# Performance work log

Hardware: AMD Instinct MI355X
Metric: run time of the kernel (lower is better)

The kernel has to match this reference:

```python
import jax, jax.numpy as jnp
import numpy as np

B, N_PATCH, N_TABLE, N_CLS, E, H = 2, 2048, 16, 1, 512, 8
N = N_PATCH + N_TABLE + N_CLS  # 2065
D = E // H
SCALE = D ** -0.5
EPS = 1e-6


def setup_inputs() -> dict:
    key = jax.random.key(0)
    k0, k1, k2 = jax.random.split(key, 3)
    # 0.02 weight scale keeps A_raw moderate so the module's un-shifted exp() is stable,
    # matching typical trained-weight magnitudes.
    x = jax.random.normal(k0, (B, N, E), jnp.float32)
    w_qkv = jax.random.normal(k1, (E, 3 * E), jnp.float32) * 0.02
    b_qkv = jnp.zeros((3 * E,), jnp.float32)
    w_out = jax.random.normal(k2, (E, E), jnp.float32) * 0.02
    b_out = jnp.zeros((E,), jnp.float32)
    return {"x": x, "w_qkv": w_qkv, "b_qkv": b_qkv, "w_out": w_out, "b_out": b_out}


def _balanced_attention(A_raw):
    # Segmented softmax: patch / table / cls each normalized separately (no max-shift,
    # +1e-6 in denominator — faithful to the torch source), then mixed by a 3-way
    # softmax over (patch-mean, table-mean, cls-max) segment statistics.
    Ap = A_raw[..., :N_PATCH]
    At = A_raw[..., N_PATCH:N_PATCH + N_TABLE]
    Ac = A_raw[..., N_PATCH + N_TABLE:]
    ep = jnp.exp(Ap.mean(-1, keepdims=True))
    et = jnp.exp(At.mean(-1, keepdims=True))
    ec = jnp.exp(Ac.max(-1, keepdims=True))
    s = ep + et + ec
    def seg(a, w):
        e = jnp.exp(a)
        return e / (e.sum(-1, keepdims=True) + EPS) * w
    return jnp.concatenate([seg(Ap, ep / s), seg(At, et / s), seg(Ac, ec / s)], axis=-1)


def reference(x, w_qkv, b_qkv, w_out, b_out):
    qkv = x @ w_qkv + b_qkv                       # [B, N, 3E]
    q, k, v = jnp.split(qkv, 3, axis=-1)
    to_heads = lambda t: t.reshape(B, N, H, D).transpose(0, 2, 1, 3)  # b n (h d) -> b h n d
    q, k, v = to_heads(q), to_heads(k), to_heads(v)
    A_raw = jnp.einsum('bhnd,bhmd->bhnm', q, k) * SCALE
    A = _balanced_attention(A_raw)
    # dropout is identity in eval mode
    out = jnp.einsum('bhnm,bhmd->bhnd', A, v)
    out = out.transpose(0, 2, 1, 3).reshape(B, N, E)  # b h n d -> b n (h d)
    out = out @ w_out + b_out
    return (out, A, A_raw)
```

## Files before the change

kernel.cpp:

```cpp
#include <hip/hip_runtime.h>
#include <hip/hip_bf16.h>

#define BB     2
#define NN     2065
#define NPAD   2112
#define HH     8
#define DD     64
#define EE     512
#define MROWS  (BB*NN)
#define NPATCH 2048
#define NTAB   16
#define SCALEF 0.125f
#define EPSF   1e-6f

typedef __bf16 bf16;
typedef bf16  bf16x8 __attribute__((ext_vector_type(8)));
typedef bf16  bf16x4v __attribute__((ext_vector_type(4)));
typedef float f32x4  __attribute__((ext_vector_type(4)));

#define LDS_STRIDE 72

__global__ __launch_bounds__(256) void k_zero(uint4* __restrict__ p, int n4) {
    int i = blockIdx.x * 256 + threadIdx.x;
    if (i < n4) { uint4 z = {0,0,0,0}; p[i] = z; }
}

__global__ __launch_bounds__(256) void k_cvt(const float* __restrict__ x,
                                             bf16* __restrict__ o, int n4) {
    int i = blockIdx.x * 256 + threadIdx.x;
    if (i < n4) {
        float4 v = ((const float4*)x)[i];
        bf16x4v r;
        r[0] = (bf16)v.x; r[1] = (bf16)v.y; r[2] = (bf16)v.z; r[3] = (bf16)v.w;
        *(bf16x4v*)(o + 4*(size_t)i) = r;
    }
}

__global__ __launch_bounds__(256) void k_transcvt(const float* __restrict__ w,
                                                  bf16* __restrict__ o,
                                                  int C, int total) {
    int i = blockIdx.x * 256 + threadIdx.x;
    if (i < total) {
        int k = i & 511, c = i >> 9;
        o[i] = (bf16)w[(size_t)k * C + c];
    }
}

__global__ __launch_bounds__(256) void k_gemm_qkv(
    const bf16* __restrict__ xb, const bf16* __restrict__ wt,
    const float* __restrict__ bias,
    bf16* __restrict__ Qh, bf16* __restrict__ Kh, bf16* __restrict__ Vt)
{
    __shared__ bf16 As[64][LDS_STRIDE];
    __shared__ bf16 Bs[64][LDS_STRIDE];
    int t = threadIdx.x;
    int w = t >> 6, l = t & 63, l15 = l & 15, quad = l >> 4;
    int m0 = blockIdx.y * 64, c0 = blockIdx.x * 64;
    int srow = t >> 2, sseg = (t & 3) * 16;
    f32x4 acc[4] = {};

    for (int kk = 0; kk < 512; kk += 64) {
        {
            int m = m0 + srow;
            uint4 v0 = {0,0,0,0}, v1 = {0,0,0,0};
            if (m < MROWS) {
                const uint4* src = (const uint4*)(xb + (size_t)m*512 + kk + sseg);
                v0 = src[0]; v1 = src[1];
            }
            *(uint4*)&As[srow][sseg]     = v0;
            *(uint4*)&As[srow][sseg + 8] = v1;
            const uint4* bs = (const uint4*)(wt + (size_t)(c0 + srow)*512 + kk + sseg);
            *(uint4*)&Bs[srow][sseg]     = bs[0];
            *(uint4*)&Bs[srow][sseg + 8] = bs[1];
        }
        __syncthreads();
        #pragma unroll
        for (int kh = 0; kh < 2; kh++) {
            bf16x8 a = *(const bf16x8*)&As[w*16 + l15][kh*32 + quad*8];
            #pragma unroll
            for (int c = 0; c < 4; c++) {
                bf16x8 b = *(const bf16x8*)&Bs[c*16 + l15][kh*32 + quad*8];
                acc[c] = __builtin_amdgcn_mfma_f32_16x16x32_bf16(a, b, acc[c], 0, 0, 0);
            }
        }
        __syncthreads();
    }

    int which = c0 >> 9;
    int h = (c0 & 511) >> 6;
    #pragma unroll
    for (int c = 0; c < 4; c++) {
        int d  = (c0 & 63) + c*16 + l15;
        float bv = bias[c0 + c*16 + l15];
        #pragma unroll
        for (int r = 0; r < 4; r++) {
            int m = m0 + w*16 + quad*4 + r;
            if (m >= MROWS) continue;
            int b_ = m / NN, n = m - b_ * NN;
            int bh = b_ * 8 + h;
            float v = acc[c][r] + bv;
            if (which == 0)      Qh[(size_t)(bh*NPAD + n)*64 + d] = (bf16)v;
            else if (which == 1) Kh[(size_t)(bh*NPAD + n)*64 + d] = (bf16)v;
            else                 Vt[((size_t)bh*64 + d)*NPAD + n] = (bf16)v;
        }
    }
}

__global__ __launch_bounds__(256) void k_attn1(
    const bf16* __restrict__ Qh, const bf16* __restrict__ Kh,
    float* __restrict__ Araw, float4* __restrict__ stats)
{
    __shared__ bf16 Qs[64][LDS_STRIDE];
    __shared__ bf16 Ks[64][LDS_STRIDE];
    int t = threadIdx.x;
    int w = t >> 6, l = t & 63, l15 = l & 15, quad = l >> 4;
    int n0 = blockIdx.x * 64;
    int bh = blockIdx.y;
    int srow = t >> 2, sseg = (t & 3) * 16;
    {
        const uint4* src = (const uint4*)(Qh + (size_t)(bh*NPAD + n0 + srow)*64 + sseg);
        *(uint4*)&Qs[srow][sseg]     = src[0];
        *(uint4*)&Qs[srow][sseg + 8] = src[1];
    }
    float sp[4]  = {0,0,0,0}, sep[4] = {0,0,0,0};
    float st[4]  = {0,0,0,0}, set_[4] = {0,0,0,0}, cv[4] = {0,0,0,0};
    int nrow[4];
    #pragma unroll
    for (int r = 0; r < 4; r++) nrow[r] = n0 + w*16 + quad*4 + r;

    for (int kt = 0; kt < 33; kt++) {
        __syncthreads();
        {
            const uint4* src = (const uint4*)(Kh + (size_t)(bh*NPAD + kt*64 + srow)*64 + sseg);
            *(uint4*)&Ks[srow][sseg]     = src[0];
            *(uint4*)&Ks[srow][sseg + 8] = src[1];
        }
        __syncthreads();
        f32x4 acc[4] = {};
        #pragma unroll
        for (int kh = 0; kh < 2; kh++) {
            bf16x8 a = *(const bf16x8*)&Qs[w*16 + l15][kh*32 + quad*8];
            #pragma unroll
            for (int c = 0; c < 4; c++) {
                bf16x8 b = *(const bf16x8*)&Ks[c*16 + l15][kh*32 + quad*8];
                acc[c] = __builtin_amdgcn_mfma_f32_16x16x32_bf16(a, b, acc[c], 0, 0, 0);
            }
        }
        #pragma unroll
        for (int c = 0; c < 4; c++) {
            int col = kt*64 + c*16 + l15;
            #pragma unroll
            for (int r = 0; r < 4; r++) {
                float val = acc[c][r] * SCALEF;
                float e = __expf(val);
                if (col < NPATCH)            { sp[r] += val; sep[r] += e; }
                else if (col < NPATCH+NTAB)  { st[r] += val; set_[r] += e; }
                else if (col == NPATCH+NTAB) { cv[r] = val; }
                if (col < NN && nrow[r] < NN)
                    Araw[((size_t)(bh*NN + nrow[r]))*NN + col] = val;
            }
        }
    }
    #pragma unroll
    for (int r = 0; r < 4; r++) {
        #pragma unroll
        for (int m = 1; m < 16; m <<= 1) {
            sp[r]   += __shfl_xor(sp[r],   m, 64);
            sep[r]  += __shfl_xor(sep[r],  m, 64);
            st[r]   += __shfl_xor(st[r],   m, 64);
            set_[r] += __shfl_xor(set_[r], m, 64);
            cv[r]   += __shfl_xor(cv[r],   m, 64);
        }
    }
    if (l15 == 0) {
        #pragma unroll
        for (int r = 0; r < 4; r++) {
            if (nrow[r] < NN) {
                float ep = __expf(sp[r] * (1.0f / NPATCH));
                float et = __expf(st[r] * (1.0f / NTAB));
                float ec = __expf(cv[r]);
                float s  = ep + et + ec;
                float4 o;
                o.x = ep / (s * (sep[r]  + EPSF));
                o.y = et / (s * (set_[r] + EPSF));
                o.z = ec / (s * (ec      + EPSF));
                o.w = 0.f;
                stats[bh*NPAD + nrow[r]] = o;
            }
        }
    }
}

__global__ __launch_bounds__(256) void k_attn2(
    const bf16* __restrict__ Qh, const bf16* __restrict__ Kh,
    const bf16* __restrict__ Vt, const float4* __restrict__ stats,
    float* __restrict__ A, bf16* __restrict__ attn)
{
    __shared__ bf16 Qs[64][LDS_STRIDE];
    __shared__ bf16 Ks[64][LDS_STRIDE];
    __shared__ bf16 Vs[64][LDS_STRIDE];
    __shared__ bf16 Ps[64][LDS_STRIDE];
    int t = threadIdx.x;
    int w = t >> 6, l = t & 63, l15 = l & 15, quad = l >> 4;
    int n0 = blockIdx.x * 64;
    int bh = blockIdx.y;
    int srow = t >> 2, sseg = (t & 3) * 16;
    {
        const uint4* src = (const uint4*)(Qh + (size_t)(bh*NPAD + n0 + srow)*64 + sseg);
        *(uint4*)&Qs[srow][sseg]     = src[0];
        *(uint4*)&Qs[srow][sseg + 8] = src[1];
    }
    int nrow[4];
    float cp[4], ctb[4], cc[4];
    #pragma unroll
    for (int r = 0; r < 4; r++) {
        nrow[r] = n0 + w*16 + quad*4 + r;
        float4 s4 = stats[bh*NPAD + nrow[r]];
        cp[r] = s4.x; ctb[r] = s4.y; cc[r] = s4.z;
    }
    f32x4 o[4] = {};

    for (int kt = 0; kt < 33; kt++) {
        __syncthreads();
        {
            const uint4* ks = (const uint4*)(Kh + (size_t)(bh*NPAD + kt*64 + srow)*64 + sseg);
            *(uint4*)&Ks[srow][sseg]     = ks[0];
            *(uint4*)&Ks[srow][sseg + 8] = ks[1];
            const uint4* vs = (const uint4*)(Vt + ((size_t)bh*64 + srow)*NPAD + kt*64 + sseg);
            *(uint4*)&Vs[srow][sseg]     = vs[0];
            *(uint4*)&Vs[srow][sseg + 8] = vs[1];
        }
        __syncthreads();
        f32x4 acc[4] = {};
        #pragma unroll
        for (int kh = 0; kh < 2; kh++) {
            bf16x8 a = *(const bf16x8*)&Qs[w*16 + l15][kh*32 + quad*8];
            #pragma unroll
            for (int c = 0; c < 4; c++) {
                bf16x8 b = *(const bf16x8*)&Ks[c*16 + l15][kh*32 + quad*8];
                acc[c] = __builtin_amdgcn_mfma_f32_16x16x32_bf16(a, b, acc[c], 0, 0, 0);
            }
        }
        #pragma unroll
        for (int c = 0; c < 4; c++) {
            int col = kt*64 + c*16 + l15;
            #pragma unroll
            for (int r = 0; r < 4; r++) {
                float val = acc[c][r] * SCALEF;
                float e = __expf(val);
                float coef = (col < NPATCH) ? cp[r]
                           : (col < NPATCH+NTAB) ? ctb[r]
                           : (col == NPATCH+NTAB) ? cc[r] : 0.f;
                float av = e * coef;
                if (col < NN && nrow[r] < NN)
                    A[((size_t)(bh*NN + nrow[r]))*NN + col] = av;
                Ps[w*16 + quad*4 + r][c*16 + l15] = (bf16)av;
            }
        }
        __syncthreads();
        #pragma unroll
        for (int kh = 0; kh < 2; kh++) {
            bf16x8 pa = *(const bf16x8*)&Ps[w*16 + l15][kh*32 + quad*8];
            #pragma unroll
            for (int g = 0; g < 4; g++) {
                bf16x8 vb = *(const bf16x8*)&Vs[g*16 + l15][kh*32 + quad*8];
                o[g] = __builtin_amdgcn_mfma_f32_16x16x32_bf16(pa, vb, o[g], 0, 0, 0);
            }
        }
    }
    int b_ = bh >> 3, h = bh & 7;
    #pragma unroll
    for (int g = 0; g < 4; g++) {
        #pragma unroll
        for (int r = 0; r < 4; r++) {
            int n = nrow[r];
            if (n < NN)
                attn[((size_t)(b_*NN + n))*512 + h*64 + g*16 + l15] = (bf16)o[g][r];
        }
    }
}

__global__ __launch_bounds__(256) void k_gemm_out(
    const bf16* __restrict__ attn, const bf16* __restrict__ wt,
    const float* __restrict__ bias, float* __restrict__ out)
{
    __shared__ bf16 As[64][LDS_STRIDE];
    __shared__ bf16 Bs[64][LDS_STRIDE];
    int t = threadIdx.x;
    int w = t >> 6, l = t & 63, l15 = l & 15, quad = l >> 4;
    int m0 = blockIdx.y * 64, c0 = blockIdx.x * 64;
    int srow = t >> 2, sseg = (t & 3) * 16;
    f32x4 acc[4] = {};

    for (int kk = 0; kk < 512; kk += 64) {
        {
            int m = m0 + srow;
            uint4 v0 = {0,0,0,0}, v1 = {0,0,0,0};
            if (m < MROWS) {
                const uint4* src = (const uint4*)(attn + (size_t)m*512 + kk + sseg);
                v0 = src[0]; v1 = src[1];
            }
            *(uint4*)&As[srow][sseg]     = v0;
            *(uint4*)&As[srow][sseg + 8] = v1;
            const uint4* bs = (const uint4*)(wt + (size_t)(c0 + srow)*512 + kk + sseg);
            *(uint4*)&Bs[srow][sseg]     = bs[0];
            *(uint4*)&Bs[srow][sseg + 8] = bs[1];
        }
        __syncthreads();
        #pragma unroll
        for (int kh = 0; kh < 2; kh++) {
            bf16x8 a = *(const bf16x8*)&As[w*16 + l15][kh*32 + quad*8];
            #pragma unroll
            for (int c = 0; c < 4; c++) {
                bf16x8 b = *(const bf16x8*)&Bs[c*16 + l15][kh*32 + quad*8];
                acc[c] = __builtin_amdgcn_mfma_f32_16x16x32_bf16(a, b, acc[c], 0, 0, 0);
            }
        }
        __syncthreads();
    }
    #pragma unroll
    for (int c = 0; c < 4; c++) {
        int col = c0 + c*16 + l15;
        float bv = bias[col];
        #pragma unroll
        for (int r = 0; r < 4; r++) {
            int m = m0 + w*16 + quad*4 + r;
            if (m < MROWS)
                out[(size_t)m*512 + col] = acc[c][r] + bv;
        }
    }
}

extern "C" void kernel_launch(void* const* d_in, const int* in_sizes, int n_in,
                              void* d_out, int out_size, void* d_ws, size_t ws_size,
                              hipStream_t stream)
{
    const float* x     = (const float*)d_in[0];
    const float* w_qkv = (const float*)d_in[1];
    const float* b_qkv = (const float*)d_in[2];
    const float* w_out = (const float*)d_in[3];
    const float* b_out = (const float*)d_in[4];

    float* out  = (float*)d_out;
    float* A    = out + (size_t)MROWS * 512;
    float* Araw = A   + (size_t)BB * HH * NN * NN;

    char* ws = (char*)d_ws;
    size_t off = 0;
    auto alloc = [&](size_t bytes) {
        char* p = ws + off;
        off += (bytes + 255) & ~(size_t)255;
        return p;
    };
    bf16*  xb    = (bf16*)alloc((size_t)MROWS * 512 * 2);
    bf16*  wqt   = (bf16*)alloc((size_t)1536 * 512 * 2);
    bf16*  wot   = (bf16*)alloc((size_t)512 * 512 * 2);
    bf16*  Qh    = (bf16*)alloc((size_t)16 * NPAD * 64 * 2);
    bf16*  Kh    = (bf16*)alloc((size_t)16 * NPAD * 64 * 2);
    bf16*  Vt    = (bf16*)alloc((size_t)16 * NPAD * 64 * 2);
    float4* stats = (float4*)alloc((size_t)16 * NPAD * 16);
    bf16*  attn  = (bf16*)alloc((size_t)MROWS * 512 * 2);
    (void)ws_size; (void)in_sizes; (void)n_in; (void)out_size;

    int zero4 = (int)((size_t)3 * 16 * NPAD * 64 * 2 / 16);
    k_zero<<<dim3((zero4 + 255) / 256), 256, 0, stream>>>((uint4*)Qh, zero4);

    k_cvt<<<dim3((MROWS*512/4 + 255) / 256), 256, 0, stream>>>(x, xb, MROWS*512/4);
    k_transcvt<<<dim3(1536*512/256), 256, 0, stream>>>(w_qkv, wqt, 1536, 1536*512);
    k_transcvt<<<dim3(512*512/256),  256, 0, stream>>>(w_out, wot, 512,  512*512);

    k_gemm_qkv<<<dim3(24, 65), 256, 0, stream>>>(xb, wqt, b_qkv, Qh, Kh, Vt);
    k_attn1<<<dim3(33, 16), 256, 0, stream>>>(Qh, Kh, Araw, stats);
    k_attn2<<<dim3(33, 16), 256, 0, stream>>>(Qh, Kh, Vt, stats, A, attn);
    k_gemm_out<<<dim3(8, 65), 256, 0, stream>>>(attn, wot, b_out, out);
}
```

Measured before the change: 729.7 us.

## Fuse two-pass attention into one kernel holding full score rows in registers

Merges the stats pass and the probability/PV pass into one kernel. Each block now handles 16 query rows, and each wave owns a quarter of the key range. The QK^T scores stay in registers (33 accumulators per thread), so QK^T is no longer computed twice and the stats buffer round-trip goes away. Segment statistics are reduced across waves through LDS. The normalized probabilities for the whole row are then staged in LDS, and each wave computes 16 output dims of P@V. This costs heavy register pressure and large LDS per block, and the key and value loads are per-wave with little reuse across query rows.

```diff
diff --git a/kernel.cpp b/kernel.cpp
--- a/kernel.cpp
+++ b/kernel.cpp
@@ -106,177 +106,158 @@
     }
 }
 
-__global__ __launch_bounds__(256) void k_attn1(
+__global__ __launch_bounds__(256, 2) void k_attn_fused(
     const bf16* __restrict__ Qh, const bf16* __restrict__ Kh,
-    float* __restrict__ Araw, float4* __restrict__ stats)
+    const bf16* __restrict__ Vt,
+    float* __restrict__ Araw, float* __restrict__ A,
+    bf16* __restrict__ attn)
 {
-    __shared__ bf16 Qs[64][LDS_STRIDE];
-    __shared__ bf16 Ks[64][LDS_STRIDE];
+    __shared__ bf16 Ps[16][2120];
+    __shared__ bf16 Kw[4][16][LDS_STRIDE];
+    __shared__ float sSP[4][16], sSE[4][16];
+    __shared__ float sT[16], sTE[16], sC[16];
+
     int t = threadIdx.x;
     int w = t >> 6, l = t & 63, l15 = l & 15, quad = l >> 4;
-    int n0 = blockIdx.x * 64;
+    int n0 = blockIdx.x * 16;
     int bh = blockIdx.y;
-    int srow = t >> 2, sseg = (t & 3) * 16;
-    {
-        const uint4* src = (const uint4*)(Qh + (size_t)(bh*NPAD + n0 + srow)*64 + sseg);
-        *(uint4*)&Qs[srow][sseg]     = src[0];
-        *(uint4*)&Qs[srow][sseg + 8] = src[1];
-    }
-    float sp[4]  = {0,0,0,0}, sep[4] = {0,0,0,0};
-    float st[4]  = {0,0,0,0}, set_[4] = {0,0,0,0}, cv[4] = {0,0,0,0};
-    int nrow[4];
-    #pragma unroll
-    for (int r = 0; r < 4; r++) nrow[r] = n0 + w*16 + quad*4 + r;
-
-    for (int kt = 0; kt < 33; kt++) {
-        __syncthreads();
-        {
-            const uint4* src = (const uint4*)(Kh + (size_t)(bh*NPAD + kt*64 + srow)*64 + sseg);
-            *(uint4*)&Ks[srow][sseg]     = src[0];
-            *(uint4*)&Ks[srow][sseg + 8] = src[1];
-        }
-        __syncthreads();
-        f32x4 acc[4] = {};
-        #pragma unroll
-        for (int kh = 0; kh < 2; kh++) {
-            bf16x8 a = *(const bf16x8*)&Qs[w*16 + l15][kh*32 + quad*8];
+    int lrow = l >> 2, lseg = (l & 3) * 16;
+
+    const bf16* qrow = Qh + ((size_t)bh * NPAD + n0 + l15) * 64 + quad * 8;
+    bf16x8 qa0 = *(const bf16x8*)qrow;
+    bf16x8 qa1 = *(const bf16x8*)(qrow + 32);
+
+    const bf16* kbase = Kh + ((size_t)bh * NPAD + w * 528) * 64;
+    const uint4* kp = (const uint4*)(kbase + (size_t)lrow * 64 + lseg);
+    uint4 p0 = kp[0], p1 = kp[1];
+
+    f32x4 acc[33];
+    float sp[4] = {0,0,0,0}, sep[4] = {0,0,0,0};
+    float st[4] = {0,0,0,0}, set_[4] = {0,0,0,0}, cv[4] = {0,0,0,0};
+
+    #pragma unroll
+    for (int kt = 0; kt < 33; ++kt) {
+        *(uint4*)&Kw[w][lrow][lseg]     = p0;
+        *(uint4*)&Kw[w][lrow][lseg + 8] = p1;
+        if (kt < 32) {
+            const uint4* np = (const uint4*)(kbase + ((size_t)(kt+1)*16 + lrow) * 64 + lseg);
+            p0 = np[0]; p1 = np[1];
+        }
+        bf16x8 b0 = *(const bf16x8*)&Kw[w][l15][quad*8];
+        bf16x8 b1 = *(const bf16x8*)&Kw[w][l15][32 + quad*8];
+        f32x4 c = {0,0,0,0};
+        c = __builtin_amdgcn_mfma_f32_16x16x32_bf16(qa0, b0, c, 0, 0, 0);
+        c = __builtin_amdgcn_mfma_f32_16x16x32_bf16(qa1, b1, c, 0, 0, 0);
+        #pragma unroll
+        for (int r = 0; r < 4; ++r) {
+            float val = c[r] * SCALEF;
+            c[r] = val;
+            if (w < 3 || kt <= 28)      { sp[r] += val; sep[r]  += __expf(val); }
+            else if (kt == 29)          { st[r] += val; set_[r] += __expf(val); }
+            else if (kt == 30)          { if (l15 == 0) cv[r] = val; }
+        }
+        acc[kt] = c;
+    }
+
+    #pragma unroll
+    for (int r = 0; r < 4; ++r) {
+        #pragma unroll
+        for (int m = 1; m < 16; m <<= 1) {
+            sp[r]  += __shfl_xor(sp[r],  m, 64);
+            sep[r] += __shfl_xor(sep[r], m, 64);
+        }
+    }
+    if (w == 3) {
+        #pragma unroll
+        for (int r = 0; r < 4; ++r) {
             #pragma unroll
-            for (int c = 0; c < 4; c++) {
-                bf16x8 b = *(const bf16x8*)&Ks[c*16 + l15][kh*32 + quad*8];
-                acc[c] = __builtin_amdgcn_mfma_f32_16x16x32_bf16(a, b, acc[c], 0, 0, 0);
-            }
-        }
-        #pragma unroll
-        for (int c = 0; c < 4; c++) {
-            int col = kt*64 + c*16 + l15;
-            #pragma unroll
-            for (int r = 0; r < 4; r++) {
-                float val = acc[c][r] * SCALEF;
-                float e = __expf(val);
-                if (col < NPATCH)            { sp[r] += val; sep[r] += e; }
-                else if (col < NPATCH+NTAB)  { st[r] += val; set_[r] += e; }
-                else if (col == NPATCH+NTAB) { cv[r] = val; }
-                if (col < NN && nrow[r] < NN)
-                    Araw[((size_t)(bh*NN + nrow[r]))*NN + col] = val;
-            }
-        }
-    }
-    #pragma unroll
-    for (int r = 0; r < 4; r++) {
-        #pragma unroll
-        for (int m = 1; m < 16; m <<= 1) {
-            sp[r]   += __shfl_xor(sp[r],   m, 64);
-            sep[r]  += __shfl_xor(sep[r],  m, 64);
-            st[r]   += __shfl_xor(st[r],   m, 64);
-            set_[r] += __shfl_xor(set_[r], m, 64);
-            cv[r]   += __shfl_xor(cv[r],   m, 64);
+            for (int m = 1; m < 16; m <<= 1) {
+                st[r]   += __shfl_xor(st[r],   m, 64);
+                set_[r] += __shfl_xor(set_[r], m, 64);
+                cv[r]   += __shfl_xor(cv[r],   m, 64);
+            }
         }
     }
     if (l15 == 0) {
         #pragma unroll
-        for (int r = 0; r < 4; r++) {
-            if (nrow[r] < NN) {
-                float ep = __expf(sp[r] * (1.0f / NPATCH));
-                float et = __expf(st[r] * (1.0f / NTAB));
-                float ec = __expf(cv[r]);
-                float s  = ep + et + ec;
-                float4 o;
-                o.x = ep / (s * (sep[r]  + EPSF));
-                o.y = et / (s * (set_[r] + EPSF));
-                o.z = ec / (s * (ec      + EPSF));
-                o.w = 0.f;
-                stats[bh*NPAD + nrow[r]] = o;
-            }
-        }
-    }
-}
-
-__global__ __launch_bounds__(256) void k_attn2(
-    const bf16* __restrict__ Qh, const bf16* __restrict__ Kh,
-    const bf16* __restrict__ Vt, const float4* __restrict__ stats,
-    float* __restrict__ A, bf16* __restrict__ attn)
-{
-    __shared__ bf16 Qs[64][LDS_STRIDE];
-    __shared__ bf16 Ks[64][LDS_STRIDE];
-    __shared__ bf16 Vs[64][LDS_STRIDE];
-    __shared__ bf16 Ps[64][LDS_STRIDE];
-    int t = threadIdx.x;
-    int w = t >> 6, l = t & 63, l15 = l & 15, quad = l >> 4;
-    int n0 = blockIdx.x * 64;
-    int bh = blockIdx.y;
-    int srow = t >> 2, sseg = (t & 3) * 16;
-    {
-        const uint4* src = (const uint4*)(Qh + (size_t)(bh*NPAD + n0 + srow)*64 + sseg);
-        *(uint4*)&Qs[srow][sseg]     = src[0];
-        *(uint4*)&Qs[srow][sseg + 8] = src[1];
-    }
-    int nrow[4];
-    float cp[4], ctb[4], cc[4];
-    #pragma unroll
-    for (int r = 0; r < 4; r++) {
-        nrow[r] = n0 + w*16 + quad*4 + r;
-        float4 s4 = stats[bh*NPAD + nrow[r]];
-        cp[r] = s4.x; ctb[r] = s4.y; cc[r] = s4.z;
-    }
-    f32x4 o[4] = {};
-
-    for (int kt = 0; kt < 33; kt++) {
-        __syncthreads();
-        {
-            const uint4* ks = (const uint4*)(Kh + (size_t)(bh*NPAD + kt*64 + srow)*64 + sseg);
-            *(uint4*)&Ks[srow][sseg]     = ks[0];
-            *(uint4*)&Ks[srow][sseg + 8] = ks[1];
-            const uint4* vs = (const uint4*)(Vt + ((size_t)bh*64 + srow)*NPAD + kt*64 + sseg);
-            *(uint4*)&Vs[srow][sseg]     = vs[0];
-            *(uint4*)&Vs[srow][sseg + 8] = vs[1];
-        }
-        __syncthreads();
-        f32x4 acc[4] = {};
-        #pragma unroll
-        for (int kh = 0; kh < 2; kh++) {
-            bf16x8 a = *(const bf16x8*)&Qs[w*16 + l15][kh*32 + quad*8];
-            #pragma unroll
-            for (int c = 0; c < 4; c++) {
-                bf16x8 b = *(const bf16x8*)&Ks[c*16 + l15][kh*32 + quad*8];
-                acc[c] = __builtin_amdgcn_mfma_f32_16x16x32_bf16(a, b, acc[c], 0, 0, 0);
-            }
-        }
-        #pragma unroll
-        for (int c = 0; c < 4; c++) {
-            int col = kt*64 + c*16 + l15;
-            #pragma unroll
-            for (int r = 0; r < 4; r++) {
-                float val = acc[c][r] * SCALEF;
-                float e = __expf(val);
-                float coef = (col < NPATCH) ? cp[r]
-                           : (col < NPATCH+NTAB) ? ctb[r]
-                           : (col == NPATCH+NTAB) ? cc[r] : 0.f;
-                float av = e * coef;
-                if (col < NN && nrow[r] < NN)
-                    A[((size_t)(bh*NN + nrow[r]))*NN + col] = av;
-                Ps[w*16 + quad*4 + r][c*16 + l15] = (bf16)av;
-            }
-        }
-        __syncthreads();
-        #pragma unroll
-        for (int kh = 0; kh < 2; kh++) {
-            bf16x8 pa = *(const bf16x8*)&Ps[w*16 + l15][kh*32 + quad*8];
-            #pragma unroll
-            for (int g = 0; g < 4; g++) {
-                bf16x8 vb = *(const bf16x8*)&Vs[g*16 + l15][kh*32 + quad*8];
-                o[g] = __builtin_amdgcn_mfma_f32_16x16x32_bf16(pa, vb, o[g], 0, 0, 0);
-            }
-        }
+        for (int r = 0; r < 4; ++r) {
+            sSP[w][quad*4 + r] = sp[r];
+            sSE[w][quad*4 + r] = sep[r];
+            if (w == 3) {
+                sT [quad*4 + r] = st[r];
+                sTE[quad*4 + r] = set_[r];
+                sC [quad*4 + r] = cv[r];
+            }
+        }
+    }
+    __syncthreads();
+
+    float cp[4], ct[4], cc[4];
+    #pragma unroll
+    for (int r = 0; r < 4; ++r) {
+        int row = quad*4 + r;
+        float spt  = sSP[0][row] + sSP[1][row] + sSP[2][row] + sSP[3][row];
+        float sept = sSE[0][row] + sSE[1][row] + sSE[2][row] + sSE[3][row];
+        float ep = __expf(spt * (1.0f / NPATCH));
+        float et = __expf(sT[row] * (1.0f / NTAB));
+        float ec = __expf(sC[row]);
+        float s  = ep + et + ec;
+        cp[r] = ep / (s * (sept     + EPSF));
+        ct[r] = et / (s * (sTE[row] + EPSF));
+        cc[r] = ec / (s * (ec       + EPSF));
+    }
+
+    int nvalid[4]; size_t rb[4];
+    #pragma unroll
+    for (int r = 0; r < 4; ++r) {
+        int n = n0 + quad*4 + r;
+        nvalid[r] = (n < NN);
+        rb[r] = ((size_t)(bh * NN + n)) * NN;
+    }
+    #pragma unroll
+    for (int kt = 0; kt < 33; ++kt) {
+        int colbase = w * 528 + kt * 16 + l15;
+        #pragma unroll
+        for (int r = 0; r < 4; ++r) {
+            float val = acc[kt][r];
+            float av; bool stok;
+            if (w < 3 || kt <= 28) { av = __expf(val) * cp[r]; stok = true; }
+            else if (kt == 29)     { av = __expf(val) * ct[r]; stok = true; }
+            else if (kt == 30)     { av = (l15 == 0) ? __expf(val) * cc[r] : 0.f; stok = (l15 == 0); }
+            else                   { av = 0.f; stok = false; }
+            Ps[quad*4 + r][colbase] = (bf16)av;
+            if (stok && nvalid[r]) {
+                Araw[rb[r] + colbase] = val;
+                A   [rb[r] + colbase] = av;
+            }
+        }
+    }
+    __syncthreads();
+
+    const bf16* vbase = Vt + ((size_t)bh * 64 + w * 16) * NPAD;
+    const uint4* vp = (const uint4*)(vbase + (size_t)lrow * NPAD + lseg);
+    uint4 v0 = vp[0], v1 = vp[1];
+    f32x4 o = {0,0,0,0};
+    for (int nt = 0; nt < 33; ++nt) {
+        *(uint4*)&Kw[w][lrow][lseg]     = v0;
+        *(uint4*)&Kw[w][lrow][lseg + 8] = v1;
+        if (nt < 32) {
+            const uint4* np = (const uint4*)(vbase + (size_t)lrow * NPAD + (nt+1)*64 + lseg);
+            v0 = np[0]; v1 = np[1];
+        }
+        bf16x8 pa0 = *(const bf16x8*)&Ps[l15][nt*64 + quad*8];
+        bf16x8 pa1 = *(const bf16x8*)&Ps[l15][nt*64 + 32 + quad*8];
+        bf16x8 vb0 = *(const bf16x8*)&Kw[w][l15][quad*8];
+        bf16x8 vb1 = *(const bf16x8*)&Kw[w][l15][32 + quad*8];
+        o = __builtin_amdgcn_mfma_f32_16x16x32_bf16(pa0, vb0, o, 0, 0, 0);
+        o = __builtin_amdgcn_mfma_f32_16x16x32_bf16(pa1, vb1, o, 0, 0, 0);
     }
     int b_ = bh >> 3, h = bh & 7;
     #pragma unroll
-    for (int g = 0; g < 4; g++) {
-        #pragma unroll
-        for (int r = 0; r < 4; r++) {
-            int n = nrow[r];
-            if (n < NN)
-                attn[((size_t)(b_*NN + n))*512 + h*64 + g*16 + l15] = (bf16)o[g][r];
-        }
+    for (int r = 0; r < 4; ++r) {
+        int n = n0 + quad*4 + r;
+        if (n < NN)
+            attn[((size_t)(b_ * NN + n)) * 512 + h * 64 + w * 16 + l15] = (bf16)o[r];
     }
 }
 
@@ -358,7 +339,6 @@
     bf16*  Qh    = (bf16*)alloc((size_t)16 * NPAD * 64 * 2);
     bf16*  Kh    = (bf16*)alloc((size_t)16 * NPAD * 64 * 2);
     bf16*  Vt    = (bf16*)alloc((size_t)16 * NPAD * 64 * 2);
-    float4* stats = (float4*)alloc((size_t)16 * NPAD * 16);
     bf16*  attn  = (bf16*)alloc((size_t)MROWS * 512 * 2);
     (void)ws_size; (void)in_sizes; (void)n_in; (void)out_size;
 
@@ -370,7 +350,6 @@
     k_transcvt<<<dim3(512*512/256),  256, 0, stream>>>(w_out, wot, 512,  512*512);
 
     k_gemm_qkv<<<dim3(24, 65), 256, 0, stream>>>(xb, wqt, b_qkv, Qh, Kh, Vt);
-    k_attn1<<<dim3(33, 16), 256, 0, stream>>>(Qh, Kh, Araw, stats);
-    k_attn2<<<dim3(33, 16), 256, 0, stream>>>(Qh, Kh, Vt, stats, A, attn);
+    k_attn_fused<<<dim3(130, 16), 256, 0, stream>>>(Qh, Kh, Vt, Araw, A, attn);
     k_gemm_out<<<dim3(8, 65), 256, 0, stream>>>(attn, wot, b_out, out);
 }
```

Result: slower. 818.5 us (+12.2%).

## Reuse Araw in second attention pass and load K/V fragments directly to registers

Applied to the files above, without the earlier changes.

The second attention kernel no longer recomputes QK^T. It reads the already-written fp32 Araw matrix back from global memory, exponentiates and scales it to produce A and P, and double-buffers P in LDS so each iteration needs one barrier instead of three. Both attention kernels drop LDS staging of Q/K/V and load MFMA fragments straight from global memory into registers, with software prefetch of the next tile. This trades MFMA work and barriers for an extra large fp32 read of Araw (about 136MB) plus uncoalesced register-direct loads. There is also a read-after-write dependency on Araw across kernels.

```diff
diff --git a/kernel.cpp b/kernel.cpp
--- a/kernel.cpp
+++ b/kernel.cpp
@@ -106,63 +106,76 @@
     }
 }
 
+#define A1_LOADK(dst, ktv) do {                                                    \
+    const bf16* kbn_ = kb + (size_t)(ktv)*4096;                                    \
+    _Pragma("unroll")                                                              \
+    for (int c = 0; c < 4; ++c) {                                                  \
+        dst[2*c]   = *(const bf16x8*)(kbn_ + c*1024);                              \
+        dst[2*c+1] = *(const bf16x8*)(kbn_ + c*1024 + 32);                         \
+    }                                                                              \
+} while (0)
+
+#define A1_BODY(ktv, kf) do {                                                      \
+    f32x4 acc_[4] = {};                                                            \
+    _Pragma("unroll")                                                              \
+    for (int c = 0; c < 4; ++c) {                                                  \
+        acc_[c] = __builtin_amdgcn_mfma_f32_16x16x32_bf16(qa0, kf[2*c],   acc_[c], 0, 0, 0); \
+        acc_[c] = __builtin_amdgcn_mfma_f32_16x16x32_bf16(qa1, kf[2*c+1], acc_[c], 0, 0, 0); \
+    }                                                                              \
+    _Pragma("unroll")                                                              \
+    for (int c = 0; c < 4; ++c) {                                                  \
+        int col_ = (ktv)*64 + c*16 + l15;                                          \
+        bool vc_ = col_ < NN;                                                      \
+        _Pragma("unroll")                                                          \
+        for (int r = 0; r < 4; ++r) {                                              \
+            float val_ = acc_[c][r] * SCALEF;                                      \
+            float e_ = __expf(val_);                                               \
+            if (col_ < NPATCH)            { sp[r] += val_; sep[r]  += e_; }        \
+            else if (col_ < NPATCH+NTAB)  { st[r] += val_; set_[r] += e_; }        \
+            else if (col_ == NPATCH+NTAB) { cv[r] = val_; }                        \
+            if (vc_ && vr[r]) Araw[rbase[r] + col_] = val_;                        \
+        }                                                                          \
+    }                                                                              \
+} while (0)
+
 __global__ __launch_bounds__(256) void k_attn1(
     const bf16* __restrict__ Qh, const bf16* __restrict__ Kh,
     float* __restrict__ Araw, float4* __restrict__ stats)
 {
-    __shared__ bf16 Qs[64][LDS_STRIDE];
-    __shared__ bf16 Ks[64][LDS_STRIDE];
     int t = threadIdx.x;
     int w = t >> 6, l = t & 63, l15 = l & 15, quad = l >> 4;
     int n0 = blockIdx.x * 64;
     int bh = blockIdx.y;
-    int srow = t >> 2, sseg = (t & 3) * 16;
-    {
-        const uint4* src = (const uint4*)(Qh + (size_t)(bh*NPAD + n0 + srow)*64 + sseg);
-        *(uint4*)&Qs[srow][sseg]     = src[0];
-        *(uint4*)&Qs[srow][sseg + 8] = src[1];
-    }
-    float sp[4]  = {0,0,0,0}, sep[4] = {0,0,0,0};
+
+    const bf16* qp = Qh + ((size_t)(bh*NPAD) + n0 + w*16 + l15)*64 + quad*8;
+    bf16x8 qa0 = *(const bf16x8*)qp;
+    bf16x8 qa1 = *(const bf16x8*)(qp + 32);
+
+    const bf16* kb = Kh + (size_t)(bh*NPAD)*64 + (size_t)(l15*64) + quad*8;
+
+    int nrow[4]; bool vr[4]; size_t rbase[4];
+    #pragma unroll
+    for (int r = 0; r < 4; ++r) {
+        nrow[r] = n0 + w*16 + quad*4 + r;
+        vr[r] = nrow[r] < NN;
+        rbase[r] = ((size_t)(bh*NN + nrow[r]))*NN;
+    }
+
+    float sp[4]  = {0,0,0,0}, sep[4]  = {0,0,0,0};
     float st[4]  = {0,0,0,0}, set_[4] = {0,0,0,0}, cv[4] = {0,0,0,0};
-    int nrow[4];
-    #pragma unroll
-    for (int r = 0; r < 4; r++) nrow[r] = n0 + w*16 + quad*4 + r;
-
-    for (int kt = 0; kt < 33; kt++) {
-        __syncthreads();
-        {
-            const uint4* src = (const uint4*)(Kh + (size_t)(bh*NPAD + kt*64 + srow)*64 + sseg);
-            *(uint4*)&Ks[srow][sseg]     = src[0];
-            *(uint4*)&Ks[srow][sseg + 8] = src[1];
-        }
-        __syncthreads();
-        f32x4 acc[4] = {};
-        #pragma unroll
-        for (int kh = 0; kh < 2; kh++) {
-            bf16x8 a = *(const bf16x8*)&Qs[w*16 + l15][kh*32 + quad*8];
-            #pragma unroll
-            for (int c = 0; c < 4; c++) {
-                bf16x8 b = *(const bf16x8*)&Ks[c*16 + l15][kh*32 + quad*8];
-                acc[c] = __builtin_amdgcn_mfma_f32_16x16x32_bf16(a, b, acc[c], 0, 0, 0);
-            }
-        }
-        #pragma unroll
-        for (int c = 0; c < 4; c++) {
-            int col = kt*64 + c*16 + l15;
-            #pragma unroll
-            for (int r = 0; r < 4; r++) {
-                float val = acc[c][r] * SCALEF;
-                float e = __expf(val);
-                if (col < NPATCH)            { sp[r] += val; sep[r] += e; }
-                else if (col < NPATCH+NTAB)  { st[r] += val; set_[r] += e; }
-                else if (col == NPATCH+NTAB) { cv[r] = val; }
-                if (col < NN && nrow[r] < NN)
-                    Araw[((size_t)(bh*NN + nrow[r]))*NN + col] = val;
-            }
-        }
-    }
-    #pragma unroll
-    for (int r = 0; r < 4; r++) {
+
+    bf16x8 kc[8], kn[8];
+    A1_LOADK(kc, 0);
+    for (int kt = 0; kt < 32; kt += 2) {
+        A1_LOADK(kn, kt + 1);
+        A1_BODY(kt, kc);
+        A1_LOADK(kc, kt + 2);
+        A1_BODY(kt + 1, kn);
+    }
+    A1_BODY(32, kc);
+
+    #pragma unroll
+    for (int r = 0; r < 4; ++r) {
         #pragma unroll
         for (int m = 1; m < 16; m <<= 1) {
             sp[r]   += __shfl_xor(sp[r],   m, 64);
@@ -174,7 +187,7 @@
     }
     if (l15 == 0) {
         #pragma unroll
-        for (int r = 0; r < 4; r++) {
+        for (int r = 0; r < 4; ++r) {
             if (nrow[r] < NN) {
                 float ep = __expf(sp[r] * (1.0f / NPATCH));
                 float et = __expf(st[r] * (1.0f / NTAB));
@@ -191,88 +204,91 @@
     }
 }
 
+#define A2_LOADV(dst, ktv) do {                                                    \
+    _Pragma("unroll")                                                              \
+    for (int c = 0; c < 4; ++c) {                                                  \
+        int col_ = (ktv)*64 + c*16 + l15;                                          \
+        bool vc_ = col_ < NN;                                                      \
+        _Pragma("unroll")                                                          \
+        for (int r = 0; r < 4; ++r)                                                \
+            dst[c*4+r] = (vc_ && vr[r]) ? Araw[rbase[r] + col_] : 0.f;             \
+    }                                                                              \
+} while (0)
+
+#define A2_BODY(ktv, vvv) do {                                                     \
+    int buf_ = (ktv) & 1;                                                          \
+    _Pragma("unroll")                                                              \
+    for (int c = 0; c < 4; ++c) {                                                  \
+        int col_ = (ktv)*64 + c*16 + l15;                                          \
+        bool vc_ = col_ < NN;                                                      \
+        _Pragma("unroll")                                                          \
+        for (int r = 0; r < 4; ++r) {                                              \
+            float av_ = 0.f;                                                       \
+            if (vc_ && vr[r]) {                                                    \
+                float coef_ = (col_ < NPATCH) ? cp[r]                              \
+                            : (col_ < NPATCH+NTAB) ? ct4[r] : cc4[r];              \
+                av_ = __expf(vvv[c*4+r]) * coef_;                                  \
+                A[rbase[r] + col_] = av_;                                          \
+            }                                                                      \
+            Ps[buf_][w*16 + quad*4 + r][c*16 + l15] = (bf16)av_;                   \
+        }                                                                          \
+    }                                                                              \
+    __syncthreads();                                                               \
+    {                                                                              \
+        bf16x8 pa0_ = *(const bf16x8*)&Ps[buf_][w*16 + l15][quad*8];               \
+        bf16x8 pa1_ = *(const bf16x8*)&Ps[buf_][w*16 + l15][32 + quad*8];          \
+        _Pragma("unroll")                                                          \
+        for (int g = 0; g < 4; ++g) {                                              \
+            bf16x8 v0_ = *(const bf16x8*)(vb + (size_t)(g*16)*NPAD + (ktv)*64);    \
+            bf16x8 v1_ = *(const bf16x8*)(vb + (size_t)(g*16)*NPAD + (ktv)*64 + 32); \
+            o[g] = __builtin_amdgcn_mfma_f32_16x16x32_bf16(pa0_, v0_, o[g], 0, 0, 0); \
+            o[g] = __builtin_amdgcn_mfma_f32_16x16x32_bf16(pa1_, v1_, o[g], 0, 0, 0); \
+        }                                                                          \
+    }                                                                              \
+} while (0)
+
 __global__ __launch_bounds__(256) void k_attn2(
-    const bf16* __restrict__ Qh, const bf16* __restrict__ Kh,
-    const bf16* __restrict__ Vt, const float4* __restrict__ stats,
+    const float* __restrict__ Araw, const float4* __restrict__ stats,
+    const bf16* __restrict__ Vt,
     float* __restrict__ A, bf16* __restrict__ attn)
 {
-    __shared__ bf16 Qs[64][LDS_STRIDE];
-    __shared__ bf16 Ks[64][LDS_STRIDE];
-    __shared__ bf16 Vs[64][LDS_STRIDE];
-    __shared__ bf16 Ps[64][LDS_STRIDE];
+    __shared__ bf16 Ps[2][64][LDS_STRIDE];
     int t = threadIdx.x;
     int w = t >> 6, l = t & 63, l15 = l & 15, quad = l >> 4;
     int n0 = blockIdx.x * 64;
     int bh = blockIdx.y;
-    int srow = t >> 2, sseg = (t & 3) * 16;
-    {
-        const uint4* src = (const uint4*)(Qh + (size_t)(bh*NPAD + n0 + srow)*64 + sseg);
-        *(uint4*)&Qs[srow][sseg]     = src[0];
-        *(uint4*)&Qs[srow][sseg + 8] = src[1];
-    }
-    int nrow[4];
-    float cp[4], ctb[4], cc[4];
-    #pragma unroll
-    for (int r = 0; r < 4; r++) {
+
+    int nrow[4]; bool vr[4]; size_t rbase[4];
+    float cp[4], ct4[4], cc4[4];
+    #pragma unroll
+    for (int r = 0; r < 4; ++r) {
         nrow[r] = n0 + w*16 + quad*4 + r;
-        float4 s4 = stats[bh*NPAD + nrow[r]];
-        cp[r] = s4.x; ctb[r] = s4.y; cc[r] = s4.z;
-    }
+        vr[r] = nrow[r] < NN;
+        rbase[r] = ((size_t)(bh*NN + nrow[r]))*NN;
+        float4 s4 = {0.f, 0.f, 0.f, 0.f};
+        if (vr[r]) s4 = stats[bh*NPAD + nrow[r]];
+        cp[r] = s4.x; ct4[r] = s4.y; cc4[r] = s4.z;
+    }
+
+    const bf16* vb = Vt + (size_t)(bh*64)*NPAD + (size_t)(l15)*NPAD + quad*8;
+
     f32x4 o[4] = {};
-
-    for (int kt = 0; kt < 33; kt++) {
-        __syncthreads();
-        {
-            const uint4* ks = (const uint4*)(Kh + (size_t)(bh*NPAD + kt*64 + srow)*64 + sseg);
-            *(uint4*)&Ks[srow][sseg]     = ks[0];
-            *(uint4*)&Ks[srow][sseg + 8] = ks[1];
-            const uint4* vs = (const uint4*)(Vt + ((size_t)bh*64 + srow)*NPAD + kt*64 + sseg);
-            *(uint4*)&Vs[srow][sseg]     = vs[0];
-            *(uint4*)&Vs[srow][sseg + 8] = vs[1];
-        }
-        __syncthreads();
-        f32x4 acc[4] = {};
-        #pragma unroll
-        for (int kh = 0; kh < 2; kh++) {
-            bf16x8 a = *(const bf16x8*)&Qs[w*16 + l15][kh*32 + quad*8];
-            #pragma unroll
-            for (int c = 0; c < 4; c++) {
-                bf16x8 b = *(const bf16x8*)&Ks[c*16 + l15][kh*32 + quad*8];
-                acc[c] = __builtin_amdgcn_mfma_f32_16x16x32_bf16(a, b, acc[c], 0, 0, 0);
-            }
-        }
-        #pragma unroll
-        for (int c = 0; c < 4; c++) {
-            int col = kt*64 + c*16 + l15;
-            #pragma unroll
-            for (int r = 0; r < 4; r++) {
-                float val = acc[c][r] * SCALEF;
-                float e = __expf(val);
-                float coef = (col < NPATCH) ? cp[r]
-                           : (col < NPATCH+NTAB) ? ctb[r]
-                           : (col == NPATCH+NTAB) ? cc[r] : 0.f;
-                float av = e * coef;
-                if (col < NN && nrow[r] < NN)
-                    A[((size_t)(bh*NN + nrow[r]))*NN + col] = av;
-                Ps[w*16 + quad*4 + r][c*16 + l15] = (bf16)av;
-            }
-        }
-        __syncthreads();
-        #pragma unroll
-        for (int kh = 0; kh < 2; kh++) {
-            bf16x8 pa = *(const bf16x8*)&Ps[w*16 + l15][kh*32 + quad*8];
-            #pragma unroll
-            for (int g = 0; g < 4; g++) {
-                bf16x8 vb = *(const bf16x8*)&Vs[g*16 + l15][kh*32 + quad*8];
-                o[g] = __builtin_amdgcn_mfma_f32_16x16x32_bf16(pa, vb, o[g], 0, 0, 0);
-            }
-        }
-    }
+    float vv[16], nv[16];
+
+    A2_LOADV(vv, 0);
+    for (int kt = 0; kt < 32; kt += 2) {
+        A2_LOADV(nv, kt + 1);
+        A2_BODY(kt, vv);
+        A2_LOADV(vv, kt + 2);
+        A2_BODY(kt + 1, nv);
+    }
+    A2_BODY(32, vv);
+
     int b_ = bh >> 3, h = bh & 7;
     #pragma unroll
-    for (int g = 0; g < 4; g++) {
-        #pragma unroll
-        for (int r = 0; r < 4; r++) {
+    for (int g = 0; g < 4; ++g) {
+        #pragma unroll
+        for (int r = 0; r < 4; ++r) {
             int n = nrow[r];
             if (n < NN)
                 attn[((size_t)(b_*NN + n))*512 + h*64 + g*16 + l15] = (bf16)o[g][r];
@@ -371,6 +387,6 @@
 
     k_gemm_qkv<<<dim3(24, 65), 256, 0, stream>>>(xb, wqt, b_qkv, Qh, Kh, Vt);
     k_attn1<<<dim3(33, 16), 256, 0, stream>>>(Qh, Kh, Araw, stats);
-    k_attn2<<<dim3(33, 16), 256, 0, stream>>>(Qh, Kh, Vt, stats, A, attn);
+    k_attn2<<<dim3(33, 16), 256, 0, stream>>>(Araw, stats, Vt, A, attn);
     k_gemm_out<<<dim3(8, 65), 256, 0, stream>>>(attn, wot, b_out, out);
 }
```

Result: slower. 991.2 us (+35.8%).

## Read stored raw scores in attn2 instead of recomputing QK^T, with prefetch

Applied to the files above, without the earlier changes.

The second attention pass no longer reloads Q and K or recomputes QK^T with MFMA. It reads the fp32 A_raw already written by the first pass, applies exp and the segment coefficients, and writes A. A and V tiles are register-prefetched one tile ahead to overlap global loads with compute. This trades MFMA work for an extra read of the large fp32 A_raw matrix (about 136MB). The kernel is memory-bound either way, so the net effect depends on the cache hitting the just-written A_raw.

```diff
diff --git a/kernel.cpp b/kernel.cpp
--- a/kernel.cpp
+++ b/kernel.cpp
@@ -17,6 +17,8 @@
 typedef bf16  bf16x8 __attribute__((ext_vector_type(8)));
 typedef bf16  bf16x4v __attribute__((ext_vector_type(4)));
 typedef float f32x4  __attribute__((ext_vector_type(4)));
+
+struct __attribute__((packed, aligned(4))) f4p { float v[4]; };
 
 #define LDS_STRIDE 72
 
@@ -192,70 +194,104 @@
 }
 
 __global__ __launch_bounds__(256) void k_attn2(
-    const bf16* __restrict__ Qh, const bf16* __restrict__ Kh,
-    const bf16* __restrict__ Vt, const float4* __restrict__ stats,
+    const float* __restrict__ Araw, const float4* __restrict__ stats,
+    const bf16* __restrict__ Vt,
     float* __restrict__ A, bf16* __restrict__ attn)
 {
-    __shared__ bf16 Qs[64][LDS_STRIDE];
-    __shared__ bf16 Ks[64][LDS_STRIDE];
+    __shared__ bf16 Ps[64][LDS_STRIDE];
     __shared__ bf16 Vs[64][LDS_STRIDE];
-    __shared__ bf16 Ps[64][LDS_STRIDE];
+    __shared__ float sCp[64], sCt[64], sCc[64];
+
     int t = threadIdx.x;
     int w = t >> 6, l = t & 63, l15 = l & 15, quad = l >> 4;
     int n0 = blockIdx.x * 64;
     int bh = blockIdx.y;
-    int srow = t >> 2, sseg = (t & 3) * 16;
-    {
-        const uint4* src = (const uint4*)(Qh + (size_t)(bh*NPAD + n0 + srow)*64 + sseg);
-        *(uint4*)&Qs[srow][sseg]     = src[0];
-        *(uint4*)&Qs[srow][sseg + 8] = src[1];
-    }
-    int nrow[4];
-    float cp[4], ctb[4], cc[4];
-    #pragma unroll
-    for (int r = 0; r < 4; r++) {
-        nrow[r] = n0 + w*16 + quad*4 + r;
-        float4 s4 = stats[bh*NPAD + nrow[r]];
-        cp[r] = s4.x; ctb[r] = s4.y; cc[r] = s4.z;
-    }
+    int pr = t >> 2;
+    int ps = (t & 3) * 16;
+
+    if (t < 64) {
+        bool v = (n0 + t) < NN;
+        float4 s4 = {0.f, 0.f, 0.f, 0.f};
+        if (v) s4 = stats[bh*NPAD + n0 + t];
+        sCp[t] = v ? s4.x : 0.f;
+        sCt[t] = v ? s4.y : 0.f;
+        sCc[t] = v ? s4.z : 0.f;
+    }
+    __syncthreads();
+    float cpr = sCp[pr], ctr = sCt[pr], ccr = sCc[pr];
+
+    bool prv = (n0 + pr) < NN;
+    size_t arow = ((size_t)(bh*NN) + n0 + pr) * NN;
+    const bf16* vrow = Vt + ((size_t)(bh*64) + pr) * NPAD;
+
+#define LOAD_A(dst, ktv) do {                                                  \
+    _Pragma("unroll")                                                          \
+    for (int j = 0; j < 4; ++j) {                                              \
+        int c0_ = (ktv)*64 + ps + j*4;                                         \
+        f4p v_ = {{0.f, 0.f, 0.f, 0.f}};                                       \
+        if (prv) {                                                             \
+            if (c0_ + 3 < NN) v_ = *(const f4p*)(Araw + arow + c0_);           \
+            else {                                                             \
+                if (c0_     < NN) v_.v[0] = Araw[arow + c0_];                  \
+                if (c0_ + 1 < NN) v_.v[1] = Araw[arow + c0_ + 1];              \
+                if (c0_ + 2 < NN) v_.v[2] = Araw[arow + c0_ + 2];              \
+                if (c0_ + 3 < NN) v_.v[3] = Araw[arow + c0_ + 3];              \
+            }                                                                  \
+        }                                                                      \
+        dst[j] = v_;                                                           \
+    }                                                                          \
+} while (0)
+
+#define LOAD_V(dst, ktv) do {                                                  \
+    const uint4* vp_ = (const uint4*)(vrow + (ktv)*64 + ps);                   \
+    dst[0] = vp_[0]; dst[1] = vp_[1];                                          \
+} while (0)
+
+#define STAGE_PA(a4v, ktv) do {                                                \
+    bf16x8 pb0_, pb1_;                                                         \
+    _Pragma("unroll")                                                          \
+    for (int j = 0; j < 4; ++j) {                                              \
+        int c0_ = (ktv)*64 + ps + j*4;                                         \
+        f4p av_;                                                               \
+        _Pragma("unroll")                                                      \
+        for (int e = 0; e < 4; ++e) {                                          \
+            int c_ = c0_ + e;                                                  \
+            float coef_ = (c_ < NPATCH) ? cpr                                  \
+                        : (c_ < NPATCH+NTAB) ? ctr                             \
+                        : (c_ == NPATCH+NTAB) ? ccr : 0.f;                     \
+            float a_ = __expf(a4v[j].v[e]) * coef_;                            \
+            av_.v[e] = a_;                                                     \
+            if (j < 2) pb0_[j*4+e] = (bf16)a_;                                 \
+            else       pb1_[(j-2)*4+e] = (bf16)a_;                             \
+        }                                                                      \
+        if (prv) {                                                             \
+            if (c0_ + 3 < NN) *(f4p*)(A + arow + c0_) = av_;                   \
+            else {                                                             \
+                if (c0_     < NN) A[arow + c0_    ] = av_.v[0];                \
+                if (c0_ + 1 < NN) A[arow + c0_ + 1] = av_.v[1];                \
+                if (c0_ + 2 < NN) A[arow + c0_ + 2] = av_.v[2];                \
+                if (c0_ + 3 < NN) A[arow + c0_ + 3] = av_.v[3];                \
+            }                                                                  \
+        }                                                                      \
+    }                                                                          \
+    *(bf16x8*)&Ps[pr][ps]     = pb0_;                                          \
+    *(bf16x8*)&Ps[pr][ps + 8] = pb1_;                                          \
+} while (0)
+
     f32x4 o[4] = {};
-
-    for (int kt = 0; kt < 33; kt++) {
-        __syncthreads();
-        {
-            const uint4* ks = (const uint4*)(Kh + (size_t)(bh*NPAD + kt*64 + srow)*64 + sseg);
-            *(uint4*)&Ks[srow][sseg]     = ks[0];
-            *(uint4*)&Ks[srow][sseg + 8] = ks[1];
-            const uint4* vs = (const uint4*)(Vt + ((size_t)bh*64 + srow)*NPAD + kt*64 + sseg);
-            *(uint4*)&Vs[srow][sseg]     = vs[0];
-            *(uint4*)&Vs[srow][sseg + 8] = vs[1];
-        }
-        __syncthreads();
-        f32x4 acc[4] = {};
-        #pragma unroll
-        for (int kh = 0; kh < 2; kh++) {
-            bf16x8 a = *(const bf16x8*)&Qs[w*16 + l15][kh*32 + quad*8];
-            #pragma unroll
-            for (int c = 0; c < 4; c++) {
-                bf16x8 b = *(const bf16x8*)&Ks[c*16 + l15][kh*32 + quad*8];
-                acc[c] = __builtin_amdgcn_mfma_f32_16x16x32_bf16(a, b, acc[c], 0, 0, 0);
-            }
-        }
-        #pragma unroll
-        for (int c = 0; c < 4; c++) {
-            int col = kt*64 + c*16 + l15;
-            #pragma unroll
-            for (int r = 0; r < 4; r++) {
-                float val = acc[c][r] * SCALEF;
-                float e = __expf(val);
-                float coef = (col < NPATCH) ? cp[r]
-                           : (col < NPATCH+NTAB) ? ctb[r]
-                           : (col == NPATCH+NTAB) ? cc[r] : 0.f;
-                float av = e * coef;
-                if (col < NN && nrow[r] < NN)
-                    A[((size_t)(bh*NN + nrow[r]))*NN + col] = av;
-                Ps[w*16 + quad*4 + r][c*16 + l15] = (bf16)av;
-            }
+    f4p   a4[4];
+    uint4 v4[2];
+    LOAD_A(a4, 0);
+    LOAD_V(v4, 0);
+
+    #pragma unroll 1
+    for (int kt = 0; kt < 33; ++kt) {
+        *(uint4*)&Vs[pr][ps]     = v4[0];
+        *(uint4*)&Vs[pr][ps + 8] = v4[1];
+        STAGE_PA(a4, kt);
+        if (kt < 32) {
+            LOAD_A(a4, kt + 1);
+            LOAD_V(v4, kt + 1);
         }
         __syncthreads();
         #pragma unroll
@@ -267,17 +303,22 @@
                 o[g] = __builtin_amdgcn_mfma_f32_16x16x32_bf16(pa, vb, o[g], 0, 0, 0);
             }
         }
-    }
+        __syncthreads();
+    }
+
     int b_ = bh >> 3, h = bh & 7;
     #pragma unroll
-    for (int g = 0; g < 4; g++) {
-        #pragma unroll
-        for (int r = 0; r < 4; r++) {
-            int n = nrow[r];
+    for (int g = 0; g < 4; ++g) {
+        #pragma unroll
+        for (int r = 0; r < 4; ++r) {
+            int n = n0 + w*16 + quad*4 + r;
             if (n < NN)
                 attn[((size_t)(b_*NN + n))*512 + h*64 + g*16 + l15] = (bf16)o[g][r];
         }
     }
+#undef LOAD_A
+#undef LOAD_V
+#undef STAGE_PA
 }
 
 __global__ __launch_bounds__(256) void k_gemm_out(
@@ -371,6 +412,6 @@
 
     k_gemm_qkv<<<dim3(24, 65), 256, 0, stream>>>(xb, wqt, b_qkv, Qh, Kh, Vt);
     k_attn1<<<dim3(33, 16), 256, 0, stream>>>(Qh, Kh, Araw, stats);
-    k_attn2<<<dim3(33, 16), 256, 0, stream>>>(Qh, Kh, Vt, stats, A, attn);
+    k_attn2<<<dim3(33, 16), 256, 0, stream>>>(Araw, stats, Vt, A, attn);
     k_gemm_out<<<dim3(8, 65), 256, 0, stream>>>(attn, wot, b_out, out);
 }
```

Measured after the change: 988.6 us. 35.5% more time.
